# Kernel tuning notes

Measured on AMD Instinct MI355X. Metric: run time of the kernel, lower is better.

## Reference

```python
import jax, jax.numpy as jnp
import numpy as np

B, F, D_IN, H, OUT = 32768, 200, 5, 15, 30

def setup_inputs() -> dict:
    key = jax.random.key(0)
    ks = jax.random.split(key, 7)
    return {
        "y":  jax.random.normal(ks[0], (B, F, D_IN), dtype=jnp.float32),
        "W1": jax.random.normal(ks[1], (F, D_IN, H), dtype=jnp.float32) * 0.3,
        "b1": jax.random.normal(ks[2], (F, H), dtype=jnp.float32) * 0.1,
        "W2": jax.random.normal(ks[3], (F, H, OUT), dtype=jnp.float32) * 0.2,
        "b2": jax.random.normal(ks[4], (F, OUT), dtype=jnp.float32) * 0.1,
        "W3": jax.random.normal(ks[5], (F * OUT, 1), dtype=jnp.float32) * 0.02,
        "b3": jax.random.normal(ks[6], (1,), dtype=jnp.float32) * 0.1,
    }

def reference(y, W1, b1, W2, b2, W3, b3):
    # 200 independent tiny 2-layer MLPs, batched over the feature axis f.
    # Note: original applies ReLU only AFTER the second Linear.
    h1 = jnp.einsum('bfi,fih->bfh', y, W1) + b1          # [B, F, H]
    h2 = jax.nn.relu(jnp.einsum('bfh,fho->bfo', h1, W2) + b2)  # [B, F, OUT]
    flat = h2.reshape(h2.shape[0], -1)                   # concat along feature axis -> [B, F*OUT]
    return flat @ W3 + b3                                # [B, 1]
```

## Files before the change

### kernel.cpp

```cpp
#include <hip/hip_runtime.h>

#define B_TOTAL 32768
#define NF 200
#define D_IN 5
#define NH 15
#define NOUT 30
#define RECS 216

typedef float v2f __attribute__((ext_vector_type(2)));
typedef float v4f __attribute__((ext_vector_type(4)));

__global__ __launch_bounds__(256) void precompute_kernel(
    const float* __restrict__ W1, const float* __restrict__ b1,
    const float* __restrict__ W2, const float* __restrict__ b2,
    const float* __restrict__ W3, float* __restrict__ rec)
{
    const int f = blockIdx.x;
    const int t = threadIdx.x;
    float* r = rec + f * RECS;
    if (t < NOUT) {
        const int o = t;
        float s = b2[f * NOUT + o];
        #pragma unroll
        for (int h = 0; h < NH; ++h)
            s = fmaf(b1[f * NH + h], W2[(f * NH + h) * NOUT + o], s);
        r[o] = s;
    } else if (t < 2 * NOUT) {
        const int o = t - NOUT;
        r[NOUT + o] = W3[f * NOUT + o];
    } else if (t < 2 * NOUT + D_IN * NOUT) {
        const int j = t - 2 * NOUT;
        const int i = j / NOUT;
        const int o = j - i * NOUT;
        float s = 0.f;
        #pragma unroll
        for (int h = 0; h < NH; ++h)
            s = fmaf(W1[(f * D_IN + i) * NH + h], W2[(f * NH + h) * NOUT + o], s);
        r[2 * NOUT + i * NOUT + o] = s;
    }
}

#define BTILE 64
#define NSUB 10
#define FSUB 20
#define NCHUNK 5

__global__ __launch_bounds__(640, 5) void mlp_kernel(
    const float* __restrict__ y, const float* __restrict__ rec,
    const float* __restrict__ b3, float* __restrict__ out)
{
    __shared__ float red[BTILE * NSUB];

    const int tid   = threadIdx.x;
    const int lane  = tid & 63;
    const int sub   = tid >> 6;
    const int sub_u = __builtin_amdgcn_readfirstlane(sub);
    const int b0    = blockIdx.x * BTILE;
    const int b     = b0 + lane;

    const v4f* __restrict__ yq =
        (const v4f*)(y + (size_t)b * (NF * D_IN) + sub_u * (FSUB * D_IN));
    const float* __restrict__ wrec = rec + (size_t)sub_u * FSUB * RECS;

    v2f acc0 = (v2f)0.0f, acc1 = (v2f)0.0f;

    #pragma unroll 1
    for (int cc = 0; cc < NCHUNK; ++cc) {
        v4f yv[5];
        #pragma unroll
        for (int j = 0; j < 5; ++j) yv[j] = yq[cc * 5 + j];

        #pragma unroll
        for (int k = 0; k < 4; ++k) {
            const float* __restrict__ r  = wrec + (cc * 4 + k) * RECS;
            const v2f* __restrict__ rb   = (const v2f*)r;
            const v2f* __restrict__ rw3  = (const v2f*)(r + NOUT);
            const v2f* __restrict__ rw   = (const v2f*)(r + 2 * NOUT);

            v2f z[15];
            {
                const int e = k * 5;
                const float y0 = yv[e >> 2][e & 3];
                #pragma unroll
                for (int p = 0; p < 15; ++p) z[p] = rb[p] + y0 * rw[p];
            }
            #pragma unroll
            for (int i = 1; i < D_IN; ++i) {
                const int e = k * 5 + i;
                const float yi = yv[e >> 2][e & 3];
                #pragma unroll
                for (int p = 0; p < 15; ++p) z[p] += yi * rw[i * 15 + p];
            }
            #pragma unroll
            for (int p = 0; p < 15; ++p) {
                v2f zr = __builtin_elementwise_max(z[p], (v2f)0.0f);
                if (p & 1) acc1 += zr * rw3[p];
                else       acc0 += zr * rw3[p];
            }
        }
    }

    v2f accs = acc0 + acc1;
    red[lane * NSUB + sub] = accs.x + accs.y;
    __syncthreads();

    if (tid < BTILE) {
        float s = b3[0];
        #pragma unroll
        for (int k = 0; k < NSUB; ++k) s += red[tid * NSUB + k];
        out[b0 + tid] = s;
    }
}

extern "C" void kernel_launch(void* const* d_in, const int* in_sizes, int n_in,
                              void* d_out, int out_size, void* d_ws, size_t ws_size,
                              hipStream_t stream) {
    const float* y  = (const float*)d_in[0];
    const float* W1 = (const float*)d_in[1];
    const float* b1 = (const float*)d_in[2];
    const float* W2 = (const float*)d_in[3];
    const float* b2 = (const float*)d_in[4];
    const float* W3 = (const float*)d_in[5];
    const float* b3 = (const float*)d_in[6];
    float* out = (float*)d_out;

    float* rec = (float*)d_ws;

    precompute_kernel<<<NF, 256, 0, stream>>>(W1, b1, W2, b2, W3, rec);
    mlp_kernel<<<B_TOTAL / BTILE, BTILE * NSUB, 0, stream>>>(y, rec, b3, out);
}
```

Before: 229.4 us.

## Use fp16 MFMA for per-feature fused layer with 2D grid and atomic reduction

The compute kernel is rebuilt so the folded per-feature linear map (W1·W2 plus bias, padded to K=8 with a ones column) runs on 16x16x32 fp16 MFMA instructions. Per-feature weights are masked to a block-diagonal form via a zero buffer, and y is staged into shared memory as fp16. The grid is split over feature partitions, with results combined through atomicAdd into a zeroed output. The aim is to move the FMA-bound work onto matrix cores, at the cost of fp16 precision loss, wasted MFMA lanes on zero blocks, extra memsets and atomics.

New measurement: 214.9 us. 6.3% less time.

```diff
diff --git a/kernel.cpp b/kernel.cpp
--- a/kernel.cpp
+++ b/kernel.cpp
@@ -5,110 +5,157 @@
 #define D_IN 5
 #define NH 15
 #define NOUT 30
-#define RECS 216
 
-typedef float v2f __attribute__((ext_vector_type(2)));
-typedef float v4f __attribute__((ext_vector_type(4)));
+typedef _Float16 half8 __attribute__((ext_vector_type(8)));
+typedef _Float16 half4_t __attribute__((ext_vector_type(4)));
+typedef float f32x4 __attribute__((ext_vector_type(4)));
+
+#define WS_BC_BYTES 102400
+#define WS_TOTAL (102400 + 30720)
 
 __global__ __launch_bounds__(256) void precompute_kernel(
     const float* __restrict__ W1, const float* __restrict__ b1,
     const float* __restrict__ W2, const float* __restrict__ b2,
-    const float* __restrict__ W3, float* __restrict__ rec)
+    const float* __restrict__ W3, _Float16* __restrict__ Bc,
+    float* __restrict__ w3T)
 {
-    const int f = blockIdx.x;
-    const int t = threadIdx.x;
-    float* r = rec + f * RECS;
-    if (t < NOUT) {
-        const int o = t;
-        float s = b2[f * NOUT + o];
-        #pragma unroll
-        for (int h = 0; h < NH; ++h)
-            s = fmaf(b1[f * NH + h], W2[(f * NH + h) * NOUT + o], s);
-        r[o] = s;
-    } else if (t < 2 * NOUT) {
-        const int o = t - NOUT;
-        r[NOUT + o] = W3[f * NOUT + o];
-    } else if (t < 2 * NOUT + D_IN * NOUT) {
-        const int j = t - 2 * NOUT;
-        const int i = j / NOUT;
-        const int o = j - i * NOUT;
+    const int idx = blockIdx.x * 256 + threadIdx.x;
+    if (idx >= NF * 32) return;
+    const int f  = idx >> 5;
+    const int r  = idx & 31;
+    const int hf = r >> 4;
+    const int n  = r & 15;
+    const int o  = hf * 16 + n;
+    if (o >= NOUT) return;
+
+    float bcv = b2[f * NOUT + o];
+    #pragma unroll
+    for (int h = 0; h < NH; ++h)
+        bcv = fmaf(b1[f * NH + h], W2[(f * NH + h) * NOUT + o], bcv);
+    float wc[D_IN];
+    #pragma unroll
+    for (int i = 0; i < D_IN; ++i) {
         float s = 0.f;
         #pragma unroll
         for (int h = 0; h < NH; ++h)
             s = fmaf(W1[(f * D_IN + i) * NH + h], W2[(f * NH + h) * NOUT + o], s);
-        r[2 * NOUT + i * NOUT + o] = s;
+        wc[i] = s;
     }
+    _Float16* dst = Bc + (size_t)f * 256 + (hf * 16 + n) * 8;
+    #pragma unroll
+    for (int i = 0; i < D_IN; ++i) dst[i] = (_Float16)wc[i];
+    dst[5] = (_Float16)bcv;
+    dst[6] = (_Float16)0.f;
+    dst[7] = (_Float16)0.f;
+
+    const int p = f / 20, fl = f % 20, Kg = fl / 4, w = fl % 4;
+    w3T[((size_t)(p * 4 + w) * 16 + n) * 12 + (Kg * 2 + hf)] = W3[f * NOUT + o];
 }
 
-#define BTILE 64
-#define NSUB 10
-#define FSUB 20
-#define NCHUNK 5
+#define FPART 20
+#define NPARTS 10
 
-__global__ __launch_bounds__(640, 5) void mlp_kernel(
-    const float* __restrict__ y, const float* __restrict__ rec,
-    const float* __restrict__ b3, float* __restrict__ out)
+__global__ __launch_bounds__(256, 4) void mlp_kernel(
+    const float* __restrict__ y, const _Float16* __restrict__ Bc,
+    const float* __restrict__ w3T, const float* __restrict__ b3,
+    float* __restrict__ out)
 {
-    __shared__ float red[BTILE * NSUB];
+    __shared__ __align__(16) _Float16 sy[64 * 168];
+    __shared__ __align__(16) _Float16 sB[20 * 256];
+    __shared__ __align__(16) float    sw3[4 * 16 * 12];
+    __shared__ __align__(16) _Float16 szero[8];
 
-    const int tid   = threadIdx.x;
-    const int lane  = tid & 63;
-    const int sub   = tid >> 6;
-    const int sub_u = __builtin_amdgcn_readfirstlane(sub);
-    const int b0    = blockIdx.x * BTILE;
-    const int b     = b0 + lane;
+    const int tid = threadIdx.x;
+    const int b0  = blockIdx.x * 64;
+    const int p   = blockIdx.y;
+    const int f0  = p * FPART;
 
-    const v4f* __restrict__ yq =
-        (const v4f*)(y + (size_t)b * (NF * D_IN) + sub_u * (FSUB * D_IN));
-    const float* __restrict__ wrec = rec + (size_t)sub_u * FSUB * RECS;
+    if (tid < 8) szero[tid] = (_Float16)0.f;
+    {
+        const f32x4* g = (const f32x4*)(Bc + (size_t)f0 * 256);
+        f32x4* s = (f32x4*)sB;
+        s[tid]       = g[tid];
+        s[tid + 256] = g[tid + 256];
+        if (tid < 128) s[tid + 512] = g[tid + 512];
+    }
+    if (tid < 192) ((f32x4*)sw3)[tid] = ((const f32x4*)w3T)[(size_t)p * 192 + tid];
+    #pragma unroll
+    for (int it = 0; it < 5; ++it) {
+        const int id = tid + it * 256;
+        const int b  = id / 20;
+        const int fl = id - b * 20;
+        const float* src = y + (size_t)(b0 + b) * (NF * D_IN) + (size_t)(f0 + fl) * 5;
+        const float v0 = src[0], v1 = src[1], v2 = src[2], v3 = src[3], v4 = src[4];
+        half4_t h0, h1;
+        h0[0] = (_Float16)v0; h0[1] = (_Float16)v1;
+        h0[2] = (_Float16)v2; h0[3] = (_Float16)v3;
+        h1[0] = (_Float16)v4; h1[1] = (_Float16)1.0f;
+        h1[2] = (_Float16)0.f; h1[3] = (_Float16)0.f;
+        *(half4_t*)&sy[b * 168 + fl * 8]     = h0;
+        *(half4_t*)&sy[b * 168 + fl * 8 + 4] = h1;
+    }
+    __syncthreads();
 
-    v2f acc0 = (v2f)0.0f, acc1 = (v2f)0.0f;
+    const int lane = tid & 63;
+    const int w    = tid >> 6;
+    const int n    = lane & 15;
+    const int q    = lane >> 4;
+
+    float acc[4][4];
+    #pragma unroll
+    for (int Mt = 0; Mt < 4; ++Mt)
+        #pragma unroll
+        for (int g = 0; g < 4; ++g) acc[Mt][g] = 0.f;
 
     #pragma unroll 1
-    for (int cc = 0; cc < NCHUNK; ++cc) {
-        v4f yv[5];
+    for (int Kg = 0; Kg < 5; ++Kg) {
+        const int fl = Kg * 4 + w;
+        half8 A[4];
         #pragma unroll
-        for (int j = 0; j < 5; ++j) yv[j] = yq[cc * 5 + j];
+        for (int Mt = 0; Mt < 4; ++Mt)
+            A[Mt] = *(const half8*)&sy[(Mt * 16 + n) * 168 + (Kg * 4 + q) * 8];
+
+        const _Float16* bp0 = (q == w) ? &sB[fl * 256 + n * 8]       : szero;
+        const _Float16* bp1 = (q == w) ? &sB[fl * 256 + (16 + n) * 8] : szero;
+        const half8 Bf0 = *(const half8*)bp0;
+        const half8 Bf1 = *(const half8*)bp1;
+
+        const float* w3p = &sw3[(w * 16 + n) * 12 + Kg * 2];
+        const float w30 = w3p[0], w31 = w3p[1];
 
         #pragma unroll
-        for (int k = 0; k < 4; ++k) {
-            const float* __restrict__ r  = wrec + (cc * 4 + k) * RECS;
-            const v2f* __restrict__ rb   = (const v2f*)r;
-            const v2f* __restrict__ rw3  = (const v2f*)(r + NOUT);
-            const v2f* __restrict__ rw   = (const v2f*)(r + 2 * NOUT);
-
-            v2f z[15];
-            {
-                const int e = k * 5;
-                const float y0 = yv[e >> 2][e & 3];
-                #pragma unroll
-                for (int p = 0; p < 15; ++p) z[p] = rb[p] + y0 * rw[p];
-            }
+        for (int Mt = 0; Mt < 4; ++Mt) {
+            f32x4 c0 = {0.f, 0.f, 0.f, 0.f};
+            f32x4 c1 = {0.f, 0.f, 0.f, 0.f};
+            c0 = __builtin_amdgcn_mfma_f32_16x16x32_f16(A[Mt], Bf0, c0, 0, 0, 0);
+            c1 = __builtin_amdgcn_mfma_f32_16x16x32_f16(A[Mt], Bf1, c1, 0, 0, 0);
             #pragma unroll
-            for (int i = 1; i < D_IN; ++i) {
-                const int e = k * 5 + i;
-                const float yi = yv[e >> 2][e & 3];
-                #pragma unroll
-                for (int p = 0; p < 15; ++p) z[p] += yi * rw[i * 15 + p];
-            }
-            #pragma unroll
-            for (int p = 0; p < 15; ++p) {
-                v2f zr = __builtin_elementwise_max(z[p], (v2f)0.0f);
-                if (p & 1) acc1 += zr * rw3[p];
-                else       acc0 += zr * rw3[p];
-            }
+            for (int g = 0; g < 4; ++g)
+                acc[Mt][g] += fmaxf(c0[g], 0.f) * w30 + fmaxf(c1[g], 0.f) * w31;
         }
     }
 
-    v2f accs = acc0 + acc1;
-    red[lane * NSUB + sub] = accs.x + accs.y;
-    __syncthreads();
-
-    if (tid < BTILE) {
-        float s = b3[0];
+    #pragma unroll
+    for (int Mt = 0; Mt < 4; ++Mt)
         #pragma unroll
-        for (int k = 0; k < NSUB; ++k) s += red[tid * NSUB + k];
-        out[b0 + tid] = s;
+        for (int g = 0; g < 4; ++g) {
+            float v = acc[Mt][g];
+            v += __shfl_xor(v, 1, 16);
+            v += __shfl_xor(v, 2, 16);
+            v += __shfl_xor(v, 4, 16);
+            v += __shfl_xor(v, 8, 16);
+            acc[Mt][g] = v;
+        }
+    if (n == 0) {
+        #pragma unroll
+        for (int Mt = 0; Mt < 4; ++Mt)
+            #pragma unroll
+            for (int g = 0; g < 4; ++g) {
+                const int b = b0 + Mt * 16 + q * 4 + g;
+                float v = acc[Mt][g];
+                if (p == 0 && w == 0) v += b3[0];
+                atomicAdd(&out[b], v);
+            }
     }
 }
 
@@ -124,8 +171,11 @@
     const float* b3 = (const float*)d_in[6];
     float* out = (float*)d_out;
 
-    float* rec = (float*)d_ws;
+    _Float16* Bc  = (_Float16*)d_ws;
+    float*    w3T = (float*)((char*)d_ws + WS_BC_BYTES);
 
-    precompute_kernel<<<NF, 256, 0, stream>>>(W1, b1, W2, b2, W3, rec);
-    mlp_kernel<<<B_TOTAL / BTILE, BTILE * NSUB, 0, stream>>>(y, rec, b3, out);
+    hipMemsetAsync(out, 0, (size_t)B_TOTAL * sizeof(float), stream);
+    hipMemsetAsync(d_ws, 0, WS_TOTAL, stream);
+    precompute_kernel<<<(NF * 32 + 255) / 256, 256, 0, stream>>>(W1, b1, W2, b2, W3, Bc, w3T);
+    mlp_kernel<<<dim3(B_TOTAL / 64, NPARTS), 256, 0, stream>>>(y, Bc, w3T, b3, out);
 }
```
